# Kernel tuning notes

Hardware: AMD Instinct MI355X
Metric: run time of the kernel (lower is better)

## Reference

```python
import jax, jax.numpy as jnp
import numpy as np

N = 10000
E = 320000
F_IN = 256
HID = 64
HEADS = 8
NUM_CLASSES = 2
NEG_SLOPE = 0.2


def _glorot(key, shape):
    fan_in, fan_out = shape[0], shape[-1]
    lim = (6.0 / (fan_in + fan_out)) ** 0.5
    return jax.random.uniform(key, shape, jnp.float32, -lim, lim)


def setup_inputs() -> dict:
    key = jax.random.key(0)
    ks = jax.random.split(key, 20)
    x = jax.random.normal(ks[0], (N, F_IN), jnp.float32)
    edge_index = jax.random.randint(ks[1], (2, E), 0, N, jnp.int64)
    d = {
        "x": x,
        "edge_index": edge_index,
        # layer 1: in=256 -> heads=8, C=64, concat -> 512
        "W1": _glorot(ks[2], (F_IN, HEADS * HID)),
        "a_src1": _glorot(ks[3], (HEADS, HID)),
        "a_dst1": _glorot(ks[4], (HEADS, HID)),
        "b1": jnp.zeros((HEADS * HID,), jnp.float32),
        # layer 2: in=512 -> heads=8, C=64, concat -> 512
        "W2": _glorot(ks[5], (HEADS * HID, HEADS * HID)),
        "a_src2": _glorot(ks[6], (HEADS, HID)),
        "a_dst2": _glorot(ks[7], (HEADS, HID)),
        "b2": jnp.zeros((HEADS * HID,), jnp.float32),
        # output conv: in=512 -> heads=1, C=64, no concat
        "W3": _glorot(ks[8], (HEADS * HID, HID)),
        "a_src3": _glorot(ks[9], (1, HID)),
        "a_dst3": _glorot(ks[10], (1, HID)),
        "b3": jnp.zeros((HID,), jnp.float32),
        # classifier
        "lin_W": _glorot(ks[11], (HID, NUM_CLASSES)),
        "lin_b": jnp.zeros((NUM_CLASSES,), jnp.float32),
    }
    return d


def _gat_layer(x, src, dst, W, a_src, a_dst, b, heads, ch, concat):
    # project: [N, H, C]
    h = (x @ W).reshape(-1, heads, ch)
    alpha_src = jnp.sum(h * a_src, axis=-1)  # [N, H]
    alpha_dst = jnp.sum(h * a_dst, axis=-1)  # [N, H]
    # per-edge attention logits (edge j -> i uses src alpha of j, dst alpha of i)
    e = jax.nn.leaky_relu(alpha_src[src] + alpha_dst[dst], NEG_SLOPE)  # [E, H]
    # segment softmax over incoming edges of each destination node
    m = jax.ops.segment_max(e, dst, num_segments=N)  # [N, H]
    m = jnp.where(jnp.isfinite(m), m, 0.0)
    ex = jnp.exp(e - m[dst])
    denom = jax.ops.segment_sum(ex, dst, num_segments=N)
    alpha = ex / (denom[dst] + 1e-16)  # [E, H]
    # weighted message aggregation
    out = jax.ops.segment_sum(h[src] * alpha[:, :, None], dst, num_segments=N)  # [N, H, C]
    if concat:
        out = out.reshape(N, heads * ch)
    else:
        out = out.mean(axis=1)
    return out + b


def reference(x, edge_index, W1, a_src1, a_dst1, b1, W2, a_src2, a_dst2, b2,
              W3, a_src3, a_dst3, b3, lin_W, lin_b):
    # PyG GATConv adds self loops by default
    loop = jnp.arange(N, dtype=edge_index.dtype)
    src = jnp.concatenate([edge_index[0], loop])
    dst = jnp.concatenate([edge_index[1], loop])

    h = _gat_layer(x, src, dst, W1, a_src1, a_dst1, b1, HEADS, HID, True)
    h = jax.nn.elu(h)
    h = _gat_layer(h, src, dst, W2, a_src2, a_dst2, b2, HEADS, HID, True)
    h = jax.nn.elu(h)
    h = _gat_layer(h, src, dst, W3, a_src3, a_dst3, b3, 1, HID, False)
    logits = h @ lin_W + lin_b
    return jax.nn.log_softmax(logits, axis=1)
```

## Files before the change

kernel.cpp:

```cpp
#include <hip/hip_runtime.h>
#include <cmath>

#define NEG 0.2f

typedef __bf16 bf16x8 __attribute__((ext_vector_type(8)));
typedef float  f32x4  __attribute__((ext_vector_type(4)));

__device__ __forceinline__ void async16(const __bf16* g, __bf16* l) {
  __builtin_amdgcn_global_load_lds(
      (const __attribute__((address_space(1))) void*)g,
      (__attribute__((address_space(3))) void*)l, 16, 0, 0);
}
__device__ __forceinline__ f32x4 mfma16(bf16x8 a, bf16x8 b, f32x4 c) {
  return __builtin_amdgcn_mfma_f32_16x16x32_bf16(a, b, c, 0, 0, 0);
}

__global__ void count_kernel(const int* __restrict__ ei, int* __restrict__ counts, int E, int Nn) {
  int e = blockIdx.x * blockDim.x + threadIdx.x;
  if (e >= E + Nn) return;
  int d = (e < E) ? ei[E + e] : (e - E);
  atomicAdd(&counts[d], 1);
}

__global__ __launch_bounds__(1024) void scan_kernel(const int* __restrict__ counts,
                                                    int* __restrict__ row_ptr,
                                                    int* __restrict__ cursor,
                                                    int n, int total) {
  __shared__ int sums[1024];
  int t = threadIdx.x;
  int per = (n + 1023) >> 10;
  int base = t * per;
  int s = 0;
  for (int i = 0; i < per; ++i) { int idx = base + i; if (idx < n) s += counts[idx]; }
  sums[t] = s;
  __syncthreads();
  for (int st = 1; st < 1024; st <<= 1) {
    int v = (t >= st) ? sums[t - st] : 0;
    __syncthreads();
    sums[t] += v;
    __syncthreads();
  }
  int off = (t == 0) ? 0 : sums[t - 1];
  for (int i = 0; i < per; ++i) {
    int idx = base + i;
    if (idx < n) { row_ptr[idx] = off; cursor[idx] = off; off += counts[idx]; }
  }
  if (t == 0) row_ptr[n] = total;
}

__global__ void scatter_kernel(const int* __restrict__ ei, int* __restrict__ cursor,
                               int* __restrict__ src_sorted, int E, int Nn) {
  int e = blockIdx.x * blockDim.x + threadIdx.x;
  if (e >= E + Nn) return;
  int s, d;
  if (e < E) { s = ei[e]; d = ei[E + e]; } else { s = e - E; d = e - E; }
  int pos = atomicAdd(&cursor[d], 1);
  src_sorted[pos] = s;
}

__global__ void prep_kernel(const float* __restrict__ x, __bf16* __restrict__ xsh,
                            __bf16* __restrict__ xsl,
                            const float* __restrict__ W1, __bf16* __restrict__ W1th,
                            const float* __restrict__ W2, __bf16* __restrict__ W2th,
                            const float* __restrict__ W3, __bf16* __restrict__ W3th,
                            int* __restrict__ counts, int Nn) {
  int i = blockIdx.x * blockDim.x + threadIdx.x;
  if (i < Nn) { counts[i] = 0; return; }
  i -= Nn;
  int nx = Nn * 256;
  if (i < nx) {
    float v = x[i];
    __bf16 h = (__bf16)v;
    xsh[i] = h;
    xsl[i] = (__bf16)(v - (float)h);
    return;
  }
  i -= nx;
  if (i < 256 * 512) {
    int k = i / 512, c = i % 512;
    W1th[(size_t)c * 256 + k] = (__bf16)W1[i];
    return;
  }
  i -= 256 * 512;
  if (i < 512 * 512) {
    int k = i / 512, c = i % 512;
    W2th[(size_t)c * 512 + k] = (__bf16)W2[i];
    return;
  }
  i -= 512 * 512;
  if (i < 512 * 64) {
    int k = i / 64, c = i % 64;
    W3th[(size_t)c * 512 + k] = (__bf16)W3[i];
    return;
  }
}

template <bool ASPLIT>
__global__ __launch_bounds__(256, 4) void gemm_v3(
    const __bf16* __restrict__ Ah, const __bf16* __restrict__ Al,
    const __bf16* __restrict__ Bth,
    __bf16* __restrict__ Cb,
    const float* __restrict__ asrc, const float* __restrict__ adst,
    float* __restrict__ als, float* __restrict__ ald,
    int M, int K, int Nc, int PX) {
  __shared__ __bf16 sAh[64 * 64], sBh[128 * 64];
  __shared__ __bf16 sAl[ASPLIT ? 64 * 64 : 64];

  int p = blockIdx.x;
  int c = p & 7, j = p >> 3;
  int x = c * PX + (j >> 2);
  int y = j & 3;
  int rowBase = x * 64, colBase = y * 128;
  if (rowBase >= M) return;

  int tid = threadIdx.x;
  int lane = tid & 63, wave = tid >> 6;
  int r16 = lane & 15, koct = lane >> 4, msk = r16 & 7;

  int fa0 = tid, fa1 = 256 + tid;
  int ar0 = fa0 >> 3, ar1 = fa1 >> 3;
  int as0 = (fa0 & 7) ^ (ar0 & 7);
  int as1 = (fa1 & 7) ^ (ar1 & 7);
  size_t aoff0 = (size_t)min(rowBase + ar0, M - 1) * K + as0 * 8;
  size_t aoff1 = (size_t)min(rowBase + ar1, M - 1) * K + as1 * 8;
  size_t boff[4];
#pragma unroll
  for (int r = 0; r < 4; ++r) {
    int f = r * 256 + tid;
    int col = f >> 3;
    int s = (f & 7) ^ (col & 7);
    boff[r] = (size_t)(colBase + col) * K + s * 8;
  }
  int lb0 = (wave * 64) * 8;
  int lb1 = ((256 + wave * 64)) * 8;
  int lb2 = ((512 + wave * 64)) * 8;
  int lb3 = ((768 + wave * 64)) * 8;

  int arow = wave * 16 + r16;
  f32x4 acc[8] = {};

  for (int k0 = 0; k0 < K; k0 += 64) {
    __syncthreads();
    async16(Ah + aoff0 + k0, sAh + lb0);
    async16(Ah + aoff1 + k0, sAh + lb1);
    if (ASPLIT) {
      async16(Al + aoff0 + k0, sAl + lb0);
      async16(Al + aoff1 + k0, sAl + lb1);
    }
    async16(Bth + boff[0] + k0, sBh + lb0);
    async16(Bth + boff[1] + k0, sBh + lb1);
    async16(Bth + boff[2] + k0, sBh + lb2);
    async16(Bth + boff[3] + k0, sBh + lb3);
    __syncthreads();

#pragma unroll
    for (int kk = 0; kk < 2; ++kk) {
      int ks = ((kk * 4 + koct) ^ msk) * 8;
      bf16x8 ah = *reinterpret_cast<const bf16x8*>(sAh + arow * 64 + ks);
      bf16x8 al;
      if (ASPLIT) al = *reinterpret_cast<const bf16x8*>(sAl + arow * 64 + ks);
      bf16x8 bh[8];
#pragma unroll
      for (int fn = 0; fn < 8; ++fn)
        bh[fn] = *reinterpret_cast<const bf16x8*>(sBh + (fn * 16 + r16) * 64 + ks);
#pragma unroll
      for (int fn = 0; fn < 8; ++fn) {
        acc[fn] = mfma16(ah, bh[fn], acc[fn]);
        if (ASPLIT) acc[fn] = mfma16(al, bh[fn], acc[fn]);
      }
    }
  }

  float asv[8], adv[8];
#pragma unroll
  for (int fn = 0; fn < 8; ++fn) {
    int ai = (y * 2 + (fn >> 2)) * 64 + (fn & 3) * 16 + r16;
    asv[fn] = asrc[ai];
    adv[fn] = adst[ai];
  }
#pragma unroll
  for (int r = 0; r < 4; ++r) {
    int row = rowBase + wave * 16 + koct * 4 + r;
    float psA = 0.f, pdA = 0.f, psB = 0.f, pdB = 0.f;
#pragma unroll
    for (int fn = 0; fn < 8; ++fn) {
      float v = acc[fn][r];
      if (row < M) Cb[(size_t)row * Nc + colBase + fn * 16 + r16] = (__bf16)v;
      if (fn < 4) { psA = fmaf(v, asv[fn], psA); pdA = fmaf(v, adv[fn], pdA); }
      else        { psB = fmaf(v, asv[fn], psB); pdB = fmaf(v, adv[fn], pdB); }
    }
#pragma unroll
    for (int sft = 1; sft < 16; sft <<= 1) {
      psA += __shfl_xor(psA, sft); pdA += __shfl_xor(pdA, sft);
      psB += __shfl_xor(psB, sft); pdB += __shfl_xor(pdB, sft);
    }
    if (r16 == 0 && row < M) {
      als[(size_t)row * 8 + y * 2 + 0] = psA;
      ald[(size_t)row * 8 + y * 2 + 0] = pdA;
      als[(size_t)row * 8 + y * 2 + 1] = psB;
      ald[(size_t)row * 8 + y * 2 + 1] = pdB;
    }
  }
}

__global__ __launch_bounds__(256, 4) void gemm_v2(
    const __bf16* __restrict__ Ah,
    const __bf16* __restrict__ Bth,
    float* __restrict__ Cf,
    const float* __restrict__ asrc, const float* __restrict__ adst,
    float* __restrict__ als, float* __restrict__ ald,
    int M, int K, int Nc) {
  __shared__ __bf16 sAh[128 * 64], sBh[64 * 64];

  int x = blockIdx.x;
  int rowBase = x * 128, colBase = 0;
  if (rowBase >= M) return;

  int tid = threadIdx.x;
  int lane = tid & 63, wave = tid >> 6;
  int r16 = lane & 15, koct = lane >> 4, msk = r16 & 7;

  f32x4 acc[2][4] = {};

  for (int k0 = 0; k0 < K; k0 += 64) {
    __syncthreads();
#pragma unroll
    for (int r = 0; r < 4; ++r) {
      int flat = r * 256 + tid;
      int row = flat >> 3;
      int grow = rowBase + row;
      if (grow >= M) grow = M - 1;
      int s = (flat & 7) ^ (row & 7);
      size_t go = (size_t)grow * K + k0 + s * 8;
      int lb = (r * 256 + wave * 64) * 8;
      async16(Ah + go, sAh + lb);
    }
#pragma unroll
    for (int r = 0; r < 2; ++r) {
      int flat = r * 256 + tid;
      int col = flat >> 3;
      int s = (flat & 7) ^ (col & 7);
      size_t go = (size_t)(colBase + col) * K + k0 + s * 8;
      int lb = (r * 256 + wave * 64) * 8;
      async16(Bth + go, sBh + lb);
    }
    __syncthreads();

#pragma unroll
    for (int kk = 0; kk < 2; ++kk) {
      bf16x8 ah[2], bh[4];
#pragma unroll
      for (int fm = 0; fm < 2; ++fm) {
        int off = (wave * 32 + fm * 16 + r16) * 64 + (((kk * 4 + koct) ^ msk) * 8);
        ah[fm] = *reinterpret_cast<const bf16x8*>(sAh + off);
      }
#pragma unroll
      for (int fn = 0; fn < 4; ++fn) {
        int off = (fn * 16 + r16) * 64 + (((kk * 4 + koct) ^ msk) * 8);
        bh[fn] = *reinterpret_cast<const bf16x8*>(sBh + off);
      }
#pragma unroll
      for (int fm = 0; fm < 2; ++fm)
#pragma unroll
        for (int fn = 0; fn < 4; ++fn)
          acc[fm][fn] = mfma16(ah[fm], bh[fn], acc[fm][fn]);
    }
  }

  float asv[4], adv[4];
#pragma unroll
  for (int fn = 0; fn < 4; ++fn) {
    asv[fn] = asrc[fn * 16 + r16];
    adv[fn] = adst[fn * 16 + r16];
  }
#pragma unroll
  for (int fm = 0; fm < 2; ++fm)
#pragma unroll
    for (int r = 0; r < 4; ++r) {
      int row = rowBase + wave * 32 + fm * 16 + koct * 4 + r;
      float ps = 0.f, pd = 0.f;
#pragma unroll
      for (int fn = 0; fn < 4; ++fn) {
        float v = acc[fm][fn][r];
        ps = fmaf(v, asv[fn], ps);
        pd = fmaf(v, adv[fn], pd);
        if (row < M) Cf[(size_t)row * Nc + fn * 16 + r16] = v;
      }
#pragma unroll
      for (int sft = 1; sft < 16; sft <<= 1) {
        ps += __shfl_xor(ps, sft);
        pd += __shfl_xor(pd, sft);
      }
      if (r16 == 0 && row < M) {
        als[row] = ps;
        ald[row] = pd;
      }
    }
}

__global__ __launch_bounds__(256) void agg8_kernel(const __bf16* __restrict__ Hb,
                                                   const float* __restrict__ als,
                                                   const float* __restrict__ ald,
                                                   const float* __restrict__ bias,
                                                   const int* __restrict__ row_ptr,
                                                   const int* __restrict__ src_sorted,
                                                   __bf16* __restrict__ Oh,
                                                   int Nn) {
  int n = (blockIdx.x * 256 + threadIdx.x) >> 6;
  if (n >= Nn) return;
  int lane = threadIdx.x & 63;
  int hh = lane >> 3;
  int start = row_ptr[n], deg = row_ptr[n + 1] - start;
  float aldn = ald[n * 8 + hh];

  float acc[8] = {};
  float ssum = 0.f;
  float mrun = 0.f;
  const __bf16* hcol = Hb + lane * 8;
  for (int e0 = 0; e0 < deg; e0 += 8) {
    int idx[8];
    float lv[8];
    bf16x8 v[8];
#pragma unroll
    for (int i = 0; i < 8; ++i) {
      int e = e0 + i;
      if (e > deg - 1) e = deg - 1;
      idx[i] = src_sorted[start + e];
    }
#pragma unroll
    for (int i = 0; i < 8; ++i) lv[i] = als[idx[i] * 8 + hh];
#pragma unroll
    for (int i = 0; i < 8; ++i)
      v[i] = *reinterpret_cast<const bf16x8*>(hcol + (size_t)idx[i] * 512);
    float lm = -INFINITY;
#pragma unroll
    for (int i = 0; i < 8; ++i) {
      float l = lv[i] + aldn;
      l = l > 0.f ? l : NEG * l;
      lv[i] = l;
      lm = fmaxf(lm, l);
    }
    if (__builtin_expect(lm > mrun + 24.f, 0)) {
      float sc = __expf(mrun - lm);
      ssum *= sc;
#pragma unroll
      for (int j = 0; j < 8; ++j) acc[j] *= sc;
      mrun = lm;
    }
#pragma unroll
    for (int i = 0; i < 8; ++i) {
      float w = (e0 + i < deg) ? __expf(lv[i] - mrun) : 0.f;
      ssum += w;
#pragma unroll
      for (int j = 0; j < 8; ++j) acc[j] = fmaf(w, (float)v[i][j], acc[j]);
    }
  }

  float inv = 1.f / (ssum + 1e-16f);
  bf16x8 vh;
#pragma unroll
  for (int j = 0; j < 8; ++j) {
    float v = acc[j] * inv + bias[lane * 8 + j];
    v = v > 0.f ? v : expm1f(v);
    vh[j] = (__bf16)v;
  }
  *reinterpret_cast<bf16x8*>(Oh + (size_t)n * 512 + lane * 8) = vh;
}

__global__ __launch_bounds__(256) void agg1cls_kernel(const float* __restrict__ Hf,
                                                      const float* __restrict__ als,
                                                      const float* __restrict__ ald,
                                                      const float* __restrict__ bias,
                                                      const int* __restrict__ row_ptr,
                                                      const int* __restrict__ src_sorted,
                                                      const float* __restrict__ lw,
                                                      const float* __restrict__ lb,
                                                      float* __restrict__ out,
                                                      int Nn) {
  int n = (blockIdx.x * 256 + threadIdx.x) >> 6;
  if (n >= Nn) return;
  int lane = threadIdx.x & 63;
  int start = row_ptr[n], deg = row_ptr[n + 1] - start;
  float aldn = ald[n];

  float acc = 0.f, ssum = 0.f, mrun = 0.f;
  for (int e0 = 0; e0 < deg; e0 += 8) {
    int idx[8];
    float lv[8], hv[8];
#pragma unroll
    for (int i = 0; i < 8; ++i) {
      int e = e0 + i;
      if (e > deg - 1) e = deg - 1;
      idx[i] = src_sorted[start + e];
    }
#pragma unroll
    for (int i = 0; i < 8; ++i) lv[i] = als[idx[i]];
#pragma unroll
    for (int i = 0; i < 8; ++i) hv[i] = Hf[(size_t)idx[i] * 64 + lane];
    float lm = -INFINITY;
#pragma unroll
    for (int i = 0; i < 8; ++i) {
      float l = lv[i] + aldn;
      l = l > 0.f ? l : NEG * l;
      lv[i] = l;
      lm = fmaxf(lm, l);
    }
    if (__builtin_expect(lm > mrun + 24.f, 0)) {
      float sc = __expf(mrun - lm);
      ssum *= sc;
      acc *= sc;
      mrun = lm;
    }
#pragma unroll
    for (int i = 0; i < 8; ++i) {
      float w = (e0 + i < deg) ? __expf(lv[i] - mrun) : 0.f;
      ssum += w;
      acc = fmaf(w, hv[i], acc);
    }
  }
  float o = acc / (ssum + 1e-16f) + bias[lane];

  float p0 = o * lw[lane * 2 + 0];
  float p1 = o * lw[lane * 2 + 1];
  for (int s = 32; s; s >>= 1) {
    p0 += __shfl_xor(p0, s);
    p1 += __shfl_xor(p1, s);
  }
  if (lane == 0) {
    p0 += lb[0];
    p1 += lb[1];
    float mx = fmaxf(p0, p1);
    float lse = mx + logf(expf(p0 - mx) + expf(p1 - mx));
    out[n * 2 + 0] = p0 - lse;
    out[n * 2 + 1] = p1 - lse;
  }
}

extern "C" void kernel_launch(void* const* d_in, const int* in_sizes, int n_in,
                              void* d_out, int out_size, void* d_ws, size_t ws_size,
                              hipStream_t stream) {
  (void)n_in; (void)out_size; (void)ws_size;
  const float* x     = (const float*)d_in[0];
  const int*   ei    = (const int*)d_in[1];
  const float* W1    = (const float*)d_in[2];
  const float* asrc1 = (const float*)d_in[3];
  const float* adst1 = (const float*)d_in[4];
  const float* b1    = (const float*)d_in[5];
  const float* W2    = (const float*)d_in[6];
  const float* asrc2 = (const float*)d_in[7];
  const float* adst2 = (const float*)d_in[8];
  const float* b2    = (const float*)d_in[9];
  const float* W3    = (const float*)d_in[10];
  const float* asrc3 = (const float*)d_in[11];
  const float* adst3 = (const float*)d_in[12];
  const float* b3    = (const float*)d_in[13];
  const float* linW  = (const float*)d_in[14];
  const float* linb  = (const float*)d_in[15];
  float* out = (float*)d_out;

  int Nn = in_sizes[0] / 256;
  int E  = in_sizes[1] / 2;
  int E2 = E + Nn;

  char* w = (char*)d_ws;
  auto carve = [&](size_t bytes) {
    char* p = w;
    w += (bytes + 63) & ~(size_t)63;
    return p;
  };
  __bf16* xsh  = (__bf16*)carve((size_t)Nn * 256 * 2);
  __bf16* xsl  = (__bf16*)carve((size_t)Nn * 256 * 2);
  __bf16* Ahb  = (__bf16*)carve((size_t)Nn * 512 * 2);
  __bf16* Hb16 = (__bf16*)carve((size_t)Nn * 512 * 2);
  float*  Hb3  = (float*)carve((size_t)Nn * 64 * 4);
  float*  als  = (float*)carve((size_t)Nn * 8 * 4);
  float*  ald  = (float*)carve((size_t)Nn * 8 * 4);
  __bf16* W1th = (__bf16*)carve(256 * 512 * 2);
  __bf16* W2th = (__bf16*)carve(512 * 512 * 2);
  __bf16* W3th = (__bf16*)carve(512 * 64 * 2);
  int* counts     = (int*)carve((size_t)Nn * 4);
  int* cursor     = (int*)carve((size_t)Nn * 4);
  int* row_ptr    = (int*)carve(((size_t)Nn + 1) * 4);
  int* src_sorted = (int*)carve((size_t)E2 * 4);

  int prep_total = Nn + Nn * 256 + 256 * 512 + 512 * 512 + 512 * 64;
  prep_kernel<<<(prep_total + 255) / 256, 256, 0, stream>>>(
      x, xsh, xsl, W1, W1th, W2, W2th, W3, W3th, counts, Nn);
  count_kernel<<<(E2 + 255) / 256, 256, 0, stream>>>(ei, counts, E, Nn);
  scan_kernel<<<1, 1024, 0, stream>>>(counts, row_ptr, cursor, Nn, E2);
  scatter_kernel<<<(E2 + 255) / 256, 256, 0, stream>>>(ei, cursor, src_sorted, E, Nn);

  int gx64 = (Nn + 63) / 64;
  int PX3 = (gx64 + 7) / 8;
  int nblk3 = 8 * PX3 * 4;
  int gx128 = (Nn + 127) / 128;
  int ga = (Nn + 3) / 4;

  gemm_v3<true><<<nblk3, 256, 0, stream>>>(xsh, xsl, W1th, Hb16,
                                           asrc1, adst1, als, ald, Nn, 256, 512, PX3);
  agg8_kernel<<<ga, 256, 0, stream>>>(Hb16, als, ald, b1, row_ptr, src_sorted, Ahb, Nn);
  gemm_v3<false><<<nblk3, 256, 0, stream>>>(Ahb, nullptr, W2th, Hb16,
                                            asrc2, adst2, als, ald, Nn, 512, 512, PX3);
  agg8_kernel<<<ga, 256, 0, stream>>>(Hb16, als, ald, b2, row_ptr, src_sorted, Ahb, Nn);
  gemm_v2<<<gx128, 256, 0, stream>>>(Ahb, W3th, Hb3,
                                     asrc3, adst3, als, ald, Nn, 512, 64);
  agg1cls_kernel<<<ga, 256, 0, stream>>>(Hb3, als, ald, b3, row_ptr, src_sorted,
                                         linW, linb, out, Nn);
}
```

Baseline: 207.9 us.

## Split layer-1 aggregation across heads with one wave per node-head pair

Adds agg8s_kernel, which launches eight times as many blocks, giving each head its own wave per node. Each wave processes eight edges in parallel (8 slots x 8 channel groups) and combines the partial sums with cross-lane shuffles. It uses no max-subtraction, relying on a clamped exp instead. Only the layer-1 aggregation uses the new kernel. The intent is more parallelism and better latency hiding on the gather, at the cost of redundant index and als loads per head and extra shuffle reductions.

```diff
diff --git a/kernel.cpp b/kernel.cpp
--- a/kernel.cpp
+++ b/kernel.cpp
@@ -296,6 +296,54 @@
         ald[row] = pd;
       }
     }
+}
+
+__global__ __launch_bounds__(256) void agg8s_kernel(const __bf16* __restrict__ Hb,
+                                                    const float* __restrict__ als,
+                                                    const float* __restrict__ ald,
+                                                    const float* __restrict__ bias,
+                                                    const int* __restrict__ row_ptr,
+                                                    const int* __restrict__ src_sorted,
+                                                    __bf16* __restrict__ Oh,
+                                                    int Nn) {
+  int head = blockIdx.x & 7;
+  int n = (blockIdx.x >> 3) * 4 + (threadIdx.x >> 6);
+  if (n >= Nn) return;
+  int lane = threadIdx.x & 63;
+  int slot = lane >> 3, cg = lane & 7;
+  int start = row_ptr[n], deg = row_ptr[n + 1] - start;
+  float aldn = ald[n * 8 + head];
+  const __bf16* hcol = Hb + head * 64 + cg * 8;
+
+  float acc[8] = {};
+  float ssum = 0.f;
+  for (int e0 = 0; e0 < deg; e0 += 8) {
+    int idx = src_sorted[start + min(e0 + slot, deg - 1)];
+    float l = als[idx * 8 + head] + aldn;
+    l = l > 0.f ? l : NEG * l;
+    float w = (e0 + slot < deg) ? __expf(fminf(l, 80.f)) : 0.f;
+    bf16x8 v = *reinterpret_cast<const bf16x8*>(hcol + (size_t)idx * 512);
+    ssum += w;
+#pragma unroll
+    for (int j = 0; j < 8; ++j) acc[j] = fmaf(w, (float)v[j], acc[j]);
+  }
+#pragma unroll
+  for (int s = 8; s < 64; s <<= 1) {
+    ssum += __shfl_xor(ssum, s);
+#pragma unroll
+    for (int j = 0; j < 8; ++j) acc[j] += __shfl_xor(acc[j], s);
+  }
+  if (slot == 0) {
+    float inv = 1.f / (ssum + 1e-16f);
+    bf16x8 vh;
+#pragma unroll
+    for (int j = 0; j < 8; ++j) {
+      float v = acc[j] * inv + bias[head * 64 + cg * 8 + j];
+      v = v > 0.f ? v : expm1f(v);
+      vh[j] = (__bf16)v;
+    }
+    *reinterpret_cast<bf16x8*>(Oh + (size_t)n * 512 + head * 64 + cg * 8) = vh;
+  }
 }
 
 __global__ __launch_bounds__(256) void agg8_kernel(const __bf16* __restrict__ Hb,
@@ -495,10 +543,11 @@
   int nblk3 = 8 * PX3 * 4;
   int gx128 = (Nn + 127) / 128;
   int ga = (Nn + 3) / 4;
+  int gs = ga * 8;
 
   gemm_v3<true><<<nblk3, 256, 0, stream>>>(xsh, xsl, W1th, Hb16,
                                            asrc1, adst1, als, ald, Nn, 256, 512, PX3);
-  agg8_kernel<<<ga, 256, 0, stream>>>(Hb16, als, ald, b1, row_ptr, src_sorted, Ahb, Nn);
+  agg8s_kernel<<<gs, 256, 0, stream>>>(Hb16, als, ald, b1, row_ptr, src_sorted, Ahb, Nn);
   gemm_v3<false><<<nblk3, 256, 0, stream>>>(Ahb, nullptr, W2th, Hb16,
                                             asrc2, adst2, als, ald, Nn, 512, 512, PX3);
   agg8_kernel<<<ga, 256, 0, stream>>>(Hb16, als, ald, b2, row_ptr, src_sorted, Ahb, Nn);
```

After: 232.6 us. +11.9%, slower.

## Split aggregation work so each wave handles four nodes across two heads

Applied to the files above, without the earlier changes.

The per-layer aggregation kernel no longer gives each node a full 64-lane wave covering all 8 heads. Each wave now handles 4 nodes, with 16 lanes per node covering a 2-head slice (128 columns). Consecutive block indices are interleaved so the four head slices of the same node chunks run close together, which is meant to improve L2 reuse of gathered source rows, and each gather is 256 contiguous bytes per node. In exchange the loop runs to the maximum degree among the wave's four nodes, and the index and logit loads are repeated for each of the four slices.

```diff
diff --git a/kernel.cpp b/kernel.cpp
--- a/kernel.cpp
+++ b/kernel.cpp
@@ -298,26 +298,37 @@
     }
 }
 
-__global__ __launch_bounds__(256) void agg8_kernel(const __bf16* __restrict__ Hb,
-                                                   const float* __restrict__ als,
-                                                   const float* __restrict__ ald,
-                                                   const float* __restrict__ bias,
-                                                   const int* __restrict__ row_ptr,
-                                                   const int* __restrict__ src_sorted,
-                                                   __bf16* __restrict__ Oh,
-                                                   int Nn) {
-  int n = (blockIdx.x * 256 + threadIdx.x) >> 6;
-  if (n >= Nn) return;
-  int lane = threadIdx.x & 63;
-  int hh = lane >> 3;
+__global__ __launch_bounds__(256) void agg8v4_kernel(const __bf16* __restrict__ Hb,
+                                                     const float* __restrict__ als,
+                                                     const float* __restrict__ ald,
+                                                     const float* __restrict__ bias,
+                                                     const int* __restrict__ row_ptr,
+                                                     const int* __restrict__ src_sorted,
+                                                     __bf16* __restrict__ Oh,
+                                                     int Nn) {
+  int c8 = blockIdx.x & 7;
+  int sl = c8 >> 1;
+  int chunk = (blockIdx.x >> 3) * 2 + (c8 & 1);
+  int lane = threadIdx.x & 63, wave = threadIdx.x >> 6;
+  int sub = lane >> 4;
+  int cg = lane & 15;
+  int n = chunk * 16 + wave * 4 + sub;
+  bool alive = (n < Nn);
+  if (!alive) n = Nn - 1;
+  int head = sl * 2 + (cg >> 3);
+  int colb = head * 64 + (cg & 7) * 8;
+
   int start = row_ptr[n], deg = row_ptr[n + 1] - start;
-  float aldn = ald[n * 8 + hh];
+  float aldn = ald[n * 8 + head];
+  int dm = deg;
+  dm = max(dm, __shfl_xor(dm, 16));
+  dm = max(dm, __shfl_xor(dm, 32));
 
   float acc[8] = {};
   float ssum = 0.f;
   float mrun = 0.f;
-  const __bf16* hcol = Hb + lane * 8;
-  for (int e0 = 0; e0 < deg; e0 += 8) {
+  const __bf16* hcol = Hb + colb;
+  for (int e0 = 0; e0 < dm; e0 += 8) {
     int idx[8];
     float lv[8];
     bf16x8 v[8];
@@ -328,7 +339,7 @@
       idx[i] = src_sorted[start + e];
     }
 #pragma unroll
-    for (int i = 0; i < 8; ++i) lv[i] = als[idx[i] * 8 + hh];
+    for (int i = 0; i < 8; ++i) lv[i] = als[idx[i] * 8 + head];
 #pragma unroll
     for (int i = 0; i < 8; ++i)
       v[i] = *reinterpret_cast<const bf16x8*>(hcol + (size_t)idx[i] * 512);
@@ -356,15 +367,17 @@
     }
   }
 
-  float inv = 1.f / (ssum + 1e-16f);
-  bf16x8 vh;
-#pragma unroll
-  for (int j = 0; j < 8; ++j) {
-    float v = acc[j] * inv + bias[lane * 8 + j];
-    v = v > 0.f ? v : expm1f(v);
-    vh[j] = (__bf16)v;
-  }
-  *reinterpret_cast<bf16x8*>(Oh + (size_t)n * 512 + lane * 8) = vh;
+  if (alive) {
+    float inv = 1.f / (ssum + 1e-16f);
+    bf16x8 vh;
+#pragma unroll
+    for (int j = 0; j < 8; ++j) {
+      float v = acc[j] * inv + bias[colb + j];
+      v = v > 0.f ? v : expm1f(v);
+      vh[j] = (__bf16)v;
+    }
+    *reinterpret_cast<bf16x8*>(Oh + (size_t)n * 512 + colb) = vh;
+  }
 }
 
 __global__ __launch_bounds__(256) void agg1cls_kernel(const float* __restrict__ Hf,
@@ -495,13 +508,14 @@
   int nblk3 = 8 * PX3 * 4;
   int gx128 = (Nn + 127) / 128;
   int ga = (Nn + 3) / 4;
+  int gv4 = ((Nn + 31) / 32) * 8;
 
   gemm_v3<true><<<nblk3, 256, 0, stream>>>(xsh, xsl, W1th, Hb16,
                                            asrc1, adst1, als, ald, Nn, 256, 512, PX3);
-  agg8_kernel<<<ga, 256, 0, stream>>>(Hb16, als, ald, b1, row_ptr, src_sorted, Ahb, Nn);
+  agg8v4_kernel<<<gv4, 256, 0, stream>>>(Hb16, als, ald, b1, row_ptr, src_sorted, Ahb, Nn);
   gemm_v3<false><<<nblk3, 256, 0, stream>>>(Ahb, nullptr, W2th, Hb16,
                                             asrc2, adst2, als, ald, Nn, 512, 512, PX3);
-  agg8_kernel<<<ga, 256, 0, stream>>>(Hb16, als, ald, b2, row_ptr, src_sorted, Ahb, Nn);
+  agg8v4_kernel<<<gv4, 256, 0, stream>>>(Hb16, als, ald, b2, row_ptr, src_sorted, Ahb, Nn);
   gemm_v2<<<gx128, 256, 0, stream>>>(Ahb, W3th, Hb3,
                                      asrc3, adst3, als, ald, Nn, 512, 64);
   agg1cls_kernel<<<ga, 256, 0, stream>>>(Hb3, als, ald, b3, row_ptr, src_sorted,
```

New measurement: 199.0 us (median of 2 runs). 1.04x faster.
